# Optimization experiments

Hardware: AMD Instinct MI355X
Metric: run time of the kernel (lower is better)

Reference implementation:

```python
import jax, jax.numpy as jnp
import numpy as np

N_LOWER, N_UPPER, Q_LOWER, Q_UPPER = 128, 128, 64, 64

def setup_inputs() -> dict:
    key = jax.random.key(0)
    ks = jax.random.split(key, 6)
    P = jax.random.uniform(ks[0], (64, N_LOWER, Q_LOWER), dtype=jnp.float32)
    weight = 0.1 * jax.random.normal(ks[1], (N_UPPER, N_LOWER), dtype=jnp.float32)
    bias_abs = 0.1 * jax.random.normal(ks[2], (N_UPPER, 1), dtype=jnp.float32)
    bias_q = 0.1 * jax.random.normal(ks[3], (N_UPPER, 1), dtype=jnp.float32)
    lambda_abs = 0.1 * jax.random.normal(ks[4], (N_UPPER, 1), dtype=jnp.float32)
    lambda_q = 0.1 * jax.random.normal(ks[5], (N_UPPER, 1), dtype=jnp.float32)
    return {"P": P, "weight": weight, "bias_abs": bias_abs, "bias_q": bias_q,
            "lambda_abs": lambda_abs, "lambda_q": lambda_q}

def reference(P, weight, bias_abs, bias_q, lambda_abs, lambda_q):
    # base distance kernel: D[l, m] = exp(-(m/q_lower - l/q_upper)^2)
    lower = jnp.arange(Q_LOWER, dtype=jnp.float32) / Q_LOWER          # [q_lower]
    upper = jnp.arange(Q_UPPER, dtype=jnp.float32) / Q_UPPER          # [q_upper]
    logD = -(lower[None, :] - upper[:, None]) ** 2                    # [q_upper, q_lower] = log(D)
    # T[j,k,l,m] = D[l,m] ** weight[j,k] = exp(weight[j,k] * logD[l,m])
    T = jnp.exp(weight[:, :, None, None] * logD[None, None, :, :])    # [n_up, n_low, q_up, q_low]
    # Pw[i,j,k,l] = sum_m T[j,k,l,m] * P[i,k,m]   (batched small mat-vec)
    Pw = jnp.einsum('jklm,ikm->ijkl', T, P)                           # [b, n_up, n_low, q_up]
    Pw = jnp.clip(Pw, 1e-15, 1e15)
    logsum = jnp.sum(jnp.log(Pw), axis=2)                             # [b, n_up, q_up]
    # log-domain bias: -b_q*(s0/q - lam_q)^2 - b_a*|s0/q - lam_a|
    s = jnp.arange(Q_UPPER, dtype=jnp.float32)[None, :] / Q_UPPER     # [1, q_up]
    B = -bias_q * (s - lambda_q) ** 2 - bias_abs * jnp.abs(s - lambda_abs)  # [n_up, q_up]
    return jax.nn.softmax(logsum + B[None, :, :], axis=2)             # [b, n_up, q_up]
```

## Files before the change

kernel.cpp:

```cpp
#include <hip/hip_runtime.h>


typedef _Float16 half8 __attribute__((ext_vector_type(8)));
typedef float float4v __attribute__((ext_vector_type(4)));

__global__ __launch_bounds__(256)
void drn_pack(const float* __restrict__ P, _Float16* __restrict__ pf16) {
    const int tid = blockIdx.x * 256 + threadIdx.x;
    const int ln = tid & 63;
    const int ks = (tid >> 6) & 1;
    const int it = (tid >> 7) & 3;
    const int k  = tid >> 9;
    const int i  = it * 16 + (ln & 15);
    const int m0 = ks * 32 + (ln >> 4) * 8;
    const float* src = P + ((size_t)i * 128 + k) * 64 + m0;
    half8 h;
#pragma unroll
    for (int t = 0; t < 8; ++t) h[t] = (_Float16)src[t];
    ((uint4*)pf16)[tid] = __builtin_bit_cast(uint4, h);
}

__global__ __launch_bounds__(512, 2)
void drn_fused(const _Float16* __restrict__ pf16,
               const float* __restrict__ weight,
               const float* __restrict__ bias_abs,
               const float* __restrict__ bias_q,
               const float* __restrict__ lambda_abs,
               const float* __restrict__ lambda_q,
               float* __restrict__ out) {
    __shared__ _Float16 tab[8][2][1024];
    __shared__ float red[4][64][36];

    const int tid   = threadIdx.x;
    const int lane  = tid & 63;
    const int wv    = tid >> 6;
    const int j     = blockIdx.x >> 1;
    const int ihalf = blockIdx.x & 1;

    const int la    = lane & 15;
    const int quad  = lane >> 4;
    const int rrep  = (63 - la) & 7;
    const int kbase = wv * 16;

    float wk[16];
#pragma unroll
    for (int kk = 0; kk < 16; ++kk) wk[kk] = weight[j * 128 + kbase + kk];

    float prod[8][4], logacc[8][4];
#pragma unroll
    for (int t = 0; t < 8; ++t)
#pragma unroll
        for (int q = 0; q < 4; ++q) { prod[t][q] = 1.0f; logacc[t][q] = 0.0f; }

    const float4v z4 = {0.f, 0.f, 0.f, 0.f};
    const uint4* bb = (const uint4*)pf16;
    const int boff = ihalf * 4;

    uint4 Bc[4], Bn[4];
#pragma unroll
    for (int f = 0; f < 4; ++f)
        Bc[f] = bb[(kbase * 8 + boff + f) * 64 + lane];

    const float d0 = 63.0f - (float)lane;
    const float d1 = (float)lane + 1.0f;

    {
        const float a = wk[0] * (1.0f / 4096.0f);
        const _Float16 h0 = (_Float16)__expf(-a * d0 * d0);
        const _Float16 h1 = (_Float16)__expf(-a * d1 * d1);
        _Float16* dst = tab[wv][0];
#pragma unroll
        for (int rr = 0; rr < 8; ++rr) {
            if (lane >= rr) dst[rr * 128 + lane - rr] = h0;
            dst[rr * 128 + lane + 64 - rr] = h1;
        }
    }
    __builtin_amdgcn_wave_barrier();

    for (int kk = 0; kk < 16; ++kk) {
        const _Float16* cur = tab[wv][kk & 1];
        uint4 A[8];
#pragma unroll
        for (int lt = 0; lt < 4; ++lt)
#pragma unroll
            for (int ks = 0; ks < 2; ++ks) {
                const int eb = 63 - (lt * 16 + la) + ks * 32 + quad * 8;
                A[lt * 2 + ks] = *(const uint4*)&cur[rrep * 128 + (eb - rrep)];
            }

        if (kk < 15) {
            const float a = wk[kk + 1] * (1.0f / 4096.0f);
            const _Float16 h0 = (_Float16)__expf(-a * d0 * d0);
            const _Float16 h1 = (_Float16)__expf(-a * d1 * d1);
            _Float16* dst = tab[wv][(kk + 1) & 1];
#pragma unroll
            for (int rr = 0; rr < 8; ++rr) {
                if (lane >= rr) dst[rr * 128 + lane - rr] = h0;
                dst[rr * 128 + lane + 64 - rr] = h1;
            }
        }
        __builtin_amdgcn_wave_barrier();

        if (kk < 15) {
#pragma unroll
            for (int f = 0; f < 4; ++f)
                Bn[f] = bb[((kbase + kk + 1) * 8 + boff + f) * 64 + lane];
        }

#pragma unroll
        for (int lt = 0; lt < 4; ++lt)
#pragma unroll
            for (int it = 0; it < 2; ++it) {
                float4v acc = __builtin_amdgcn_mfma_f32_16x16x32_f16(
                    __builtin_bit_cast(half8, A[lt * 2 + 0]),
                    __builtin_bit_cast(half8, Bc[it * 2 + 0]), z4, 0, 0, 0);
                acc = __builtin_amdgcn_mfma_f32_16x16x32_f16(
                    __builtin_bit_cast(half8, A[lt * 2 + 1]),
                    __builtin_bit_cast(half8, Bc[it * 2 + 1]), acc, 0, 0, 0);
#pragma unroll
                for (int q = 0; q < 4; ++q) prod[lt * 2 + it][q] *= acc[q];
            }

        if (kk == 7) {
#pragma unroll
            for (int t = 0; t < 8; ++t)
#pragma unroll
                for (int q = 0; q < 4; ++q) {
                    logacc[t][q] += __logf(prod[t][q]);
                    prod[t][q] = 1.0f;
                }
        }
        if (kk < 15) {
#pragma unroll
            for (int f = 0; f < 4; ++f) Bc[f] = Bn[f];
        }
    }
#pragma unroll
    for (int t = 0; t < 8; ++t)
#pragma unroll
        for (int q = 0; q < 4; ++q) logacc[t][q] += __logf(prod[t][q]);

    if (wv < 4) {
#pragma unroll
        for (int lt = 0; lt < 4; ++lt)
#pragma unroll
            for (int it = 0; it < 2; ++it)
#pragma unroll
                for (int q = 0; q < 4; ++q)
                    red[wv][lt * 16 + quad * 4 + q][it * 16 + la] = logacc[lt * 2 + it][q];
    }
    __syncthreads();
    if (wv >= 4) {
#pragma unroll
        for (int lt = 0; lt < 4; ++lt)
#pragma unroll
            for (int it = 0; it < 2; ++it)
#pragma unroll
                for (int q = 0; q < 4; ++q)
                    red[wv - 4][lt * 16 + quad * 4 + q][it * 16 + la] += logacc[lt * 2 + it][q];
    }
    __syncthreads();

    const float bq = bias_q[j],   lq = lambda_q[j];
    const float ba = bias_abs[j], la2 = lambda_abs[j];
    const float s  = (float)lane * (1.0f / 64.0f);
    const float dq = s - lq;
    const float Bjl = -bq * dq * dq - ba * fabsf(s - la2);

#pragma unroll
    for (int r = 0; r < 4; ++r) {
        const int il = wv * 4 + r;
        float v = red[0][lane][il] + red[1][lane][il]
                + red[2][lane][il] + red[3][lane][il] + Bjl;

        float mx = v;
#pragma unroll
        for (int off = 32; off > 0; off >>= 1)
            mx = fmaxf(mx, __shfl_xor(mx, off, 64));
        const float e = __expf(v - mx);
        float sm = e;
#pragma unroll
        for (int off = 32; off > 0; off >>= 1)
            sm += __shfl_xor(sm, off, 64);

        out[((size_t)(ihalf * 32 + il) * 128 + j) * 64 + lane] = e / sm;
    }
}

extern "C" void kernel_launch(void* const* d_in, const int* in_sizes, int n_in,
                              void* d_out, int out_size, void* d_ws, size_t ws_size,
                              hipStream_t stream) {
    const float* P          = (const float*)d_in[0];
    const float* weight     = (const float*)d_in[1];
    const float* bias_abs   = (const float*)d_in[2];
    const float* bias_q     = (const float*)d_in[3];
    const float* lambda_abs = (const float*)d_in[4];
    const float* lambda_q   = (const float*)d_in[5];
    float* outp = (float*)d_out;

    _Float16* pf16 = (_Float16*)d_ws;

    drn_pack<<<dim3(256), dim3(256), 0, stream>>>(P, pf16);
    drn_fused<<<dim3(256), dim3(512), 0, stream>>>(
        pf16, weight, bias_abs, bias_q, lambda_abs, lambda_q, outp);
}
```

Baseline: 82.72 us.

## Merge pack and compute into one cooperative kernel, reuse output as scratch

Measured after the change: 141.1 us. 1.71x slower.

```diff
diff --git a/kernel.cpp b/kernel.cpp
--- a/kernel.cpp
+++ b/kernel.cpp
@@ -1,35 +1,22 @@
 #include <hip/hip_runtime.h>
-
+#include <hip/hip_cooperative_groups.h>
+
+
+namespace cg = cooperative_groups;
 
 typedef _Float16 half8 __attribute__((ext_vector_type(8)));
 typedef float float4v __attribute__((ext_vector_type(4)));
 
-__global__ __launch_bounds__(256)
-void drn_pack(const float* __restrict__ P, _Float16* __restrict__ pf16) {
-    const int tid = blockIdx.x * 256 + threadIdx.x;
-    const int ln = tid & 63;
-    const int ks = (tid >> 6) & 1;
-    const int it = (tid >> 7) & 3;
-    const int k  = tid >> 9;
-    const int i  = it * 16 + (ln & 15);
-    const int m0 = ks * 32 + (ln >> 4) * 8;
-    const float* src = P + ((size_t)i * 128 + k) * 64 + m0;
-    half8 h;
-#pragma unroll
-    for (int t = 0; t < 8; ++t) h[t] = (_Float16)src[t];
-    ((uint4*)pf16)[tid] = __builtin_bit_cast(uint4, h);
-}
-
 __global__ __launch_bounds__(512, 2)
-void drn_fused(const _Float16* __restrict__ pf16,
-               const float* __restrict__ weight,
-               const float* __restrict__ bias_abs,
-               const float* __restrict__ bias_q,
-               const float* __restrict__ lambda_abs,
-               const float* __restrict__ lambda_q,
-               float* __restrict__ out) {
+void drn_coop(const float* __restrict__ P,
+              const float* __restrict__ weight,
+              const float* __restrict__ bias_abs,
+              const float* __restrict__ bias_q,
+              const float* __restrict__ lambda_abs,
+              const float* __restrict__ lambda_q,
+              float* __restrict__ out) {
     __shared__ _Float16 tab[8][2][1024];
-    __shared__ float red[4][64][36];
+    __shared__ float red[4][64][33];
 
     const int tid   = threadIdx.x;
     const int lane  = tid & 63;
@@ -37,6 +24,23 @@
     const int j     = blockIdx.x >> 1;
     const int ihalf = blockIdx.x & 1;
 
+    _Float16* pf16 = (_Float16*)out;
+    if (tid < 256) {
+        const int ptid = blockIdx.x * 256 + tid;
+        const int ln = ptid & 63;
+        const int ks = (ptid >> 6) & 1;
+        const int it = (ptid >> 7) & 3;
+        const int k  = ptid >> 9;
+        const int i  = it * 16 + (ln & 15);
+        const int m0 = ks * 32 + (ln >> 4) * 8;
+        const float* src = P + ((size_t)i * 128 + k) * 64 + m0;
+        half8 h;
+#pragma unroll
+        for (int t = 0; t < 8; ++t) h[t] = (_Float16)src[t];
+        ((uint4*)pf16)[ptid] = __builtin_bit_cast(uint4, h);
+    }
+    cg::this_grid().sync();
+
     const int la    = lane & 15;
     const int quad  = lane >> 4;
     const int rrep  = (63 - la) & 7;
@@ -79,14 +83,12 @@
 
     for (int kk = 0; kk < 16; ++kk) {
         const _Float16* cur = tab[wv][kk & 1];
-        uint4 A[8];
-#pragma unroll
-        for (int lt = 0; lt < 4; ++lt)
-#pragma unroll
-            for (int ks = 0; ks < 2; ++ks) {
-                const int eb = 63 - (lt * 16 + la) + ks * 32 + quad * 8;
-                A[lt * 2 + ks] = *(const uint4*)&cur[rrep * 128 + (eb - rrep)];
-            }
+        uint4 U[6];
+#pragma unroll
+        for (int u = 0; u < 6; ++u) {
+            const int eb = 63 - la + quad * 8 + 32 - 16 * u;
+            U[u] = *(const uint4*)&cur[rrep * 127 + eb];
+        }
 
         if (kk < 15) {
             const float a = wk[kk + 1] * (1.0f / 4096.0f);
@@ -112,10 +114,10 @@
 #pragma unroll
             for (int it = 0; it < 2; ++it) {
                 float4v acc = __builtin_amdgcn_mfma_f32_16x16x32_f16(
-                    __builtin_bit_cast(half8, A[lt * 2 + 0]),
+                    __builtin_bit_cast(half8, U[lt + 2]),
                     __builtin_bit_cast(half8, Bc[it * 2 + 0]), z4, 0, 0, 0);
                 acc = __builtin_amdgcn_mfma_f32_16x16x32_f16(
-                    __builtin_bit_cast(half8, A[lt * 2 + 1]),
+                    __builtin_bit_cast(half8, U[lt]),
                     __builtin_bit_cast(half8, Bc[it * 2 + 1]), acc, 0, 0, 0);
 #pragma unroll
                 for (int q = 0; q < 4; ++q) prod[lt * 2 + it][q] *= acc[q];
@@ -167,6 +169,7 @@
     const float dq = s - lq;
     const float Bjl = -bq * dq * dq - ba * fabsf(s - la2);
 
+    float res[4];
 #pragma unroll
     for (int r = 0; r < 4; ++r) {
         const int il = wv * 4 + r;
@@ -182,8 +185,14 @@
 #pragma unroll
         for (int off = 32; off > 0; off >>= 1)
             sm += __shfl_xor(sm, off, 64);
-
-        out[((size_t)(ihalf * 32 + il) * 128 + j) * 64 + lane] = e / sm;
+        res[r] = e / sm;
+    }
+
+    cg::this_grid().sync();
+#pragma unroll
+    for (int r = 0; r < 4; ++r) {
+        const int il = wv * 4 + r;
+        out[((size_t)(ihalf * 32 + il) * 128 + j) * 64 + lane] = res[r];
     }
 }
 
@@ -198,9 +207,10 @@
     const float* lambda_q   = (const float*)d_in[5];
     float* outp = (float*)d_out;
 
-    _Float16* pf16 = (_Float16*)d_ws;
-
-    drn_pack<<<dim3(256), dim3(256), 0, stream>>>(P, pf16);
-    drn_fused<<<dim3(256), dim3(512), 0, stream>>>(
-        pf16, weight, bias_abs, bias_q, lambda_abs, lambda_q, outp);
+    (void)d_ws; (void)ws_size;
+
+    void* args[] = {(void*)&P, (void*)&weight, (void*)&bias_abs, (void*)&bias_q,
+                    (void*)&lambda_abs, (void*)&lambda_q, (void*)&outp};
+    hipLaunchCooperativeKernel(reinterpret_cast<void*>(&drn_coop),
+                               dim3(256), dim3(512), args, 0u, stream);
 }
```
